# Performance work log

Hardware: AMD Instinct MI355X
Metric: run time of the kernel (lower is better)

The kernel has to match this reference:

```python
import jax, jax.numpy as jnp
import numpy as np
from jax.ops import segment_sum, segment_max

DIM = 64
NUM_FEAT = 14
EDGE_FEAT = 4
OUT_DIM = 16
NUM_GRAPHS = 512
NEG_SLOPE = 0.01


def _leaky(v):
    return jnp.where(v >= 0, v, NEG_SLOPE * v)


def setup_inputs() -> dict:
    key = jax.random.key(0)
    ks = jax.random.split(key, 24)
    N, E = 20000, 40000
    s = 0.1
    inp = {
        "x": jax.random.normal(ks[0], (N, NUM_FEAT), jnp.float32),
        "edge_attr": jax.random.normal(ks[1], (E, EDGE_FEAT), jnp.float32),
        "edge_index": jax.random.randint(ks[2], (2, E), 0, N, jnp.int64) if jax.config.jax_enable_x64 else jax.random.randint(ks[2], (2, E), 0, N).astype(jnp.int32),
        "batch": jnp.sort(jax.random.randint(ks[3], (N,), 0, NUM_GRAPHS)).astype(jnp.int32),
        # lin0
        "lin0_w": s * jax.random.normal(ks[4], (DIM, NUM_FEAT), jnp.float32),
        "lin0_b": s * jax.random.normal(ks[5], (DIM,), jnp.float32),
        # edge network: Linear(4,dim) -> LeakyReLU -> Linear(dim, dim*dim)
        "net_w1": s * jax.random.normal(ks[6], (DIM, EDGE_FEAT), jnp.float32),
        "net_b1": s * jax.random.normal(ks[7], (DIM,), jnp.float32),
        "net_w2": s * jax.random.normal(ks[8], (DIM * DIM, DIM), jnp.float32),
        "net_b2": s * jax.random.normal(ks[9], (DIM * DIM,), jnp.float32),
        # NNConv root weight + bias
        "root_w": s * jax.random.normal(ks[10], (DIM, DIM), jnp.float32),
        "conv_b": s * jax.random.normal(ks[11], (DIM,), jnp.float32),
        # GRU (torch gate order: r, z, n)
        "gru_w_ih": s * jax.random.normal(ks[12], (3 * DIM, DIM), jnp.float32),
        "gru_w_hh": s * jax.random.normal(ks[13], (3 * DIM, DIM), jnp.float32),
        "gru_b_ih": s * jax.random.normal(ks[14], (3 * DIM,), jnp.float32),
        "gru_b_hh": s * jax.random.normal(ks[15], (3 * DIM,), jnp.float32),
        # Set2Set LSTM (input 2*dim, hidden dim; torch gate order: i, f, g, o)
        "lstm_w_ih": s * jax.random.normal(ks[16], (4 * DIM, 2 * DIM), jnp.float32),
        "lstm_w_hh": s * jax.random.normal(ks[17], (4 * DIM, DIM), jnp.float32),
        "lstm_b_ih": s * jax.random.normal(ks[18], (4 * DIM,), jnp.float32),
        "lstm_b_hh": s * jax.random.normal(ks[19], (4 * DIM,), jnp.float32),
        # lin_out
        "lout_w": s * jax.random.normal(ks[20], (OUT_DIM, 2 * DIM), jnp.float32),
        "lout_b": s * jax.random.normal(ks[21], (OUT_DIM,), jnp.float32),
    }
    return inp


def _forward(x, edge_attr, lin0_w, lin0_b, net_w1, net_b1, net_w2, net_b2,
             root_w, conv_b, gru_w_ih, gru_w_hh, gru_b_ih, gru_b_hh,
             lstm_w_ih, lstm_w_hh, lstm_b_ih, lstm_b_hh, lout_w, lout_b,
             edge_index, batch):
    N = x.shape[0]
    src, tgt = edge_index[0], edge_index[1]

    # per-edge dim x dim weight (shared across the 6 steps; edge_attr is static)
    ew = _leaky(edge_attr @ net_w1.T + net_b1) @ net_w2.T + net_b2  # [E, dim*dim]
    ew = ew.reshape(-1, DIM, DIM)  # [E, in, out]

    deg = segment_sum(jnp.ones_like(tgt, jnp.float32), tgt, num_segments=N)
    inv_deg = 1.0 / jnp.maximum(deg, 1.0)

    out = _leaky(x @ lin0_w.T + lin0_b)  # [N, dim]
    h = out
    for _ in range(6):
        msg = jnp.einsum('ed,edo->eo', out[src], ew)  # gather + per-edge matvec
        agg = segment_sum(msg, tgt, num_segments=N) * inv_deg[:, None]  # scatter-mean
        conv = agg + out @ root_w + conv_b
        m = _leaky(conv)
        # GRU cell (seq len 1)
        gi = m @ gru_w_ih.T + gru_b_ih
        gh = h @ gru_w_hh.T + gru_b_hh
        gi_r, gi_z, gi_n = jnp.split(gi, 3, axis=-1)
        gh_r, gh_z, gh_n = jnp.split(gh, 3, axis=-1)
        r = jax.nn.sigmoid(gi_r + gh_r)
        z = jax.nn.sigmoid(gi_z + gh_z)
        n = jnp.tanh(gi_n + r * gh_n)
        h = (1.0 - z) * n + z * h
        out = h

    # Set2Set, processing_steps=1
    B = NUM_GRAPHS
    q_star = jnp.zeros((B, 2 * DIM), x.dtype)
    h_l = jnp.zeros((B, DIM), x.dtype)
    c_l = jnp.zeros((B, DIM), x.dtype)
    gates = q_star @ lstm_w_ih.T + lstm_b_ih + h_l @ lstm_w_hh.T + lstm_b_hh
    gi_, gf_, gg_, go_ = jnp.split(gates, 4, axis=-1)
    i_g = jax.nn.sigmoid(gi_)
    f_g = jax.nn.sigmoid(gf_)
    g_g = jnp.tanh(gg_)
    o_g = jax.nn.sigmoid(go_)
    c = f_g * c_l + i_g * g_g
    q = o_g * jnp.tanh(c)  # [B, dim]

    e = jnp.sum(out * q[batch], axis=-1)  # [N]
    emax = segment_max(e, batch, num_segments=B)
    emax = jnp.where(jnp.isfinite(emax), emax, 0.0)
    ex = jnp.exp(e - emax[batch])
    denom = segment_sum(ex, batch, num_segments=B)
    a = ex / jnp.maximum(denom, 1e-16)[batch]
    r_read = segment_sum(a[:, None] * out, batch, num_segments=B)  # [B, dim]
    q_star = jnp.concatenate([q, r_read], axis=-1)  # [B, 2*dim]

    return q_star @ lout_w.T + lout_b  # [B, out_dim]


def reference(x, edge_attr, edge_index, batch, lin0_w, lin0_b, net_w1, net_b1,
              net_w2, net_b2, root_w, conv_b, gru_w_ih, gru_w_hh, gru_b_ih,
              gru_b_hh, lstm_w_ih, lstm_w_hh, lstm_b_ih, lstm_b_hh, lout_w, lout_b):
    return _forward(x, edge_attr, lin0_w, lin0_b, net_w1, net_b1, net_w2, net_b2,
                    root_w, conv_b, gru_w_ih, gru_w_hh, gru_b_ih, gru_b_hh,
                    lstm_w_ih, lstm_w_hh, lstm_b_ih, lstm_b_hh, lout_w, lout_b,
                    edge_index, batch)
```

## Files before the change

### kernel.cpp

```cpp
#include <hip/hip_runtime.h>
#include <math.h>

#define DIM 64
#define NFEAT 14
#define EFEAT 4
#define ODIM 16
#define NGRAPH 512
#define NEG 0.01f
#define EBLK 160
#define DSPLIT 2

typedef _Float16 f16;
typedef _Float16 f16x8 __attribute__((ext_vector_type(8)));
typedef float f32x4 __attribute__((ext_vector_type(4)));

#define MFMA(a,b,c) __builtin_amdgcn_mfma_f32_16x16x32_f16(a,b,c,0,0,0)

__device__ __forceinline__ float leaky(float v){ return v >= 0.f ? v : NEG*v; }
__device__ __forceinline__ float sigm(float v){ return 1.f/(1.f+expf(-v)); }

__global__ void k_pack(const float* __restrict__ src, f16* __restrict__ dst, int NC, int transB){
    int i = blockIdx.x*blockDim.x + threadIdx.x;
    if (i >= NC*64) return;
    int j = i & 7, l = (i >> 3) & 63, s = (i >> 9) & 1, CT = i >> 10;
    int k = ((l >> 4) << 3) + 32*s + j;
    int c = CT*16 + (l & 15);
    float v = transB ? src[(size_t)k*NC + c] : src[(size_t)c*64 + k];
    dst[i] = (f16)v;
}

__global__ void k_hid(const float* __restrict__ ea, const float* __restrict__ w1,
                      const float* __restrict__ b1, f16* __restrict__ hid16, int E){
    int i = blockIdx.x*blockDim.x + threadIdx.x;
    if (i >= E*DIM) return;
    int e = i >> 6, k = i & 63;
    const float* a = ea + (size_t)e*EFEAT;
    const float* w = w1 + k*EFEAT;
    float v = b1[k] + a[0]*w[0] + a[1]*w[1] + a[2]*w[2] + a[3]*w[3];
    hid16[i] = (f16)leaky(v);
}

__global__ void k_deg(const int* __restrict__ ei, float* __restrict__ deg, int E){
    int e = blockIdx.x*blockDim.x + threadIdx.x;
    if (e < E) atomicAdd(&deg[ei[E + e]], 1.0f);
}

__global__ void k_invdeg(float* __restrict__ deg, int N){
    int i = blockIdx.x*blockDim.x + threadIdx.x;
    if (i < N) deg[i] = 1.0f / fmaxf(deg[i], 1.0f);
}

__global__ void k_lin0(const float* __restrict__ x, const float* __restrict__ w,
                       const float* __restrict__ b, float* __restrict__ hf,
                       f16* __restrict__ out16, int N){
    int i = blockIdx.x*blockDim.x + threadIdx.x;
    if (i >= N*DIM) return;
    int n = i >> 6, o = i & 63;
    const float* xr = x + (size_t)n*NFEAT;
    const float* wr = w + o*NFEAT;
    float v = b[o];
#pragma unroll
    for (int f = 0; f < NFEAT; ++f) v += xr[f]*wr[f];
    v = leaky(v);
    hf[i] = v; out16[i] = (f16)v;
}

__global__ __launch_bounds__(256) void k_nbias(const f16x8* __restrict__ out16v,
                                               const f16x8* __restrict__ b2f,
                                               float* __restrict__ nb, int N){
    int n0 = blockIdx.x*64;
    int tid = threadIdx.x, w = tid >> 6, l = tid & 63, li = l & 15, lh = l >> 4;
    int ar = n0 + 16*w + li;
    f16x8 a0{}, a1{};
    if (ar < N){ a0 = out16v[(size_t)ar*8 + lh]; a1 = out16v[(size_t)ar*8 + lh + 4]; }
    f32x4 z = {0.f,0.f,0.f,0.f};
#pragma unroll
    for (int ct = 0; ct < 4; ++ct){
        f32x4 p = MFMA(a0, b2f[(ct*2+0)*64 + l], z);
        p = MFMA(a1, b2f[(ct*2+1)*64 + l], p);
#pragma unroll
        for (int reg = 0; reg < 4; ++reg){
            int n = n0 + 16*w + lh*4 + reg;
            if (n < N) nb[(size_t)n*64 + ct*16 + li] = p[reg];
        }
    }
}

__global__ __launch_bounds__(320) void k_fmsg(const float* __restrict__ hf,
                                              const f16x8* __restrict__ hid16v,
                                              const f16x8* __restrict__ wpf,
                                              const float* __restrict__ nb,
                                              const int* __restrict__ ei,
                                              float* __restrict__ agg, int E){
    __shared__ f16x8 Wch[2][2048];
    __shared__ f16 OsT[32][168];
    __shared__ int ssrc[EBLK];
    __shared__ int stgt[EBLK];
    int tid = threadIdx.x;
    int e0 = blockIdx.x*EBLK;
    int dz = blockIdx.y;
    int dbase = dz*32;
    if (tid < EBLK){
        int e = e0 + tid;
        ssrc[tid] = (e < E) ? ei[e] : -1;
        stgt[tid] = (e < E) ? ei[E + e] : -1;
    }
    __syncthreads();
    for (int i = tid; i < EBLK*32; i += 320){
        int r = i % EBLK, dl = i / EBLK;
        int s = ssrc[r];
        OsT[dl][r] = (s >= 0) ? (f16)hf[(size_t)s*64 + dbase + dl] : (f16)0.f;
    }
    int w = tid >> 6, l = tid & 63, li = l & 15, lh = l >> 4;
    f16x8 a[2][2];
#pragma unroll
    for (int rt = 0; rt < 2; ++rt){
        int e = e0 + w*32 + rt*16 + li;
        if (e < E){
            a[rt][0] = hid16v[(size_t)e*8 + lh];
            a[rt][1] = hid16v[(size_t)e*8 + lh + 4];
        } else { a[rt][0] = f16x8{}; a[rt][1] = f16x8{}; }
    }
    {
        const f16x8* wsrc0 = wpf + (size_t)dbase*512;
        for (int i = tid; i < 2048; i += 320) Wch[0][i] = wsrc0[i];
    }
    f32x4 acc[2][4] = {};
    __syncthreads();

    for (int c = 0; c < 8; ++c){
        int cb = c & 1;
        f16x8 p0{},p1{},p2{},p3{},p4{},p5{},p6{};
        if (c < 7){
            const f16x8* src = wpf + (size_t)(dbase + (c+1)*4)*512;
            p0 = src[tid];
            p1 = src[tid + 320];
            p2 = src[tid + 640];
            p3 = src[tid + 960];
            p4 = src[tid + 1280];
            p5 = src[tid + 1600];
            if (tid < 128) p6 = src[tid + 1920];
        }
#pragma unroll
        for (int dd = 0; dd < 4; ++dd){
            int dl = c*4 + dd;
            f16 s0 = OsT[dl][w*32 + li];
            f16 s1 = OsT[dl][w*32 + 16 + li];
            f16x8 as00 = a[0][0]*s0, as01 = a[0][1]*s0;
            f16x8 as10 = a[1][0]*s1, as11 = a[1][1]*s1;
#pragma unroll
            for (int ct = 0; ct < 4; ++ct){
                f16x8 b0 = Wch[cb][(dd*8 + ct*2 + 0)*64 + l];
                f16x8 b1 = Wch[cb][(dd*8 + ct*2 + 1)*64 + l];
                acc[0][ct] = MFMA(as00, b0, acc[0][ct]);
                acc[0][ct] = MFMA(as01, b1, acc[0][ct]);
                acc[1][ct] = MFMA(as10, b0, acc[1][ct]);
                acc[1][ct] = MFMA(as11, b1, acc[1][ct]);
            }
        }
        if (c < 7){
            __syncthreads();
            int nb2 = cb ^ 1;
            Wch[nb2][tid]        = p0;
            Wch[nb2][tid + 320]  = p1;
            Wch[nb2][tid + 640]  = p2;
            Wch[nb2][tid + 960]  = p3;
            Wch[nb2][tid + 1280] = p4;
            Wch[nb2][tid + 1600] = p5;
            if (tid < 128) Wch[nb2][tid + 1920] = p6;
            __syncthreads();
        }
    }

#pragma unroll
    for (int rt = 0; rt < 2; ++rt){
#pragma unroll
        for (int reg = 0; reg < 4; ++reg){
            int row = w*32 + rt*16 + lh*4 + reg;
            int t = stgt[row];
            if (t < 0) continue;
            int s = ssrc[row];
#pragma unroll
            for (int ct = 0; ct < 4; ++ct){
                int col = ct*16 + li;
                float v = acc[rt][ct][reg];
                if (dz == 0) v += nb[(size_t)s*64 + col];
                atomicAdd(&agg[(size_t)t*64 + col], v);
            }
        }
    }
}

__global__ __launch_bounds__(256) void k_node(float* __restrict__ hf,
                                              f16* __restrict__ out16,
                                              const f16x8* __restrict__ out16v,
                                              float* __restrict__ agg,
                                              const float* __restrict__ invdeg,
                                              const float* __restrict__ convb,
                                              const f16x8* __restrict__ wrf,
                                              const f16x8* __restrict__ wihf,
                                              const f16x8* __restrict__ whhf,
                                              const float* __restrict__ bih,
                                              const float* __restrict__ bhh,
                                              const f16x8* __restrict__ b2f,
                                              float* __restrict__ nb, int N){
    __shared__ f16 Ms[64][72];
    int n0 = blockIdx.x*64;
    int tid = threadIdx.x, w = tid >> 6, l = tid & 63, li = l & 15, lh = l >> 4;
    f32x4 z = {0.f,0.f,0.f,0.f};

    int ar = n0 + 16*w + li;
    f16x8 a0{}, a1{};
    if (ar < N){ a0 = out16v[(size_t)ar*8 + lh]; a1 = out16v[(size_t)ar*8 + lh + 4]; }

    int nrow[4]; float invd[4];
#pragma unroll
    for (int reg = 0; reg < 4; ++reg){
        nrow[reg] = n0 + 16*w + lh*4 + reg;
        invd[reg] = (nrow[reg] < N) ? invdeg[nrow[reg]] : 0.f;
    }

#pragma unroll
    for (int ct = 0; ct < 4; ++ct){
        f32x4 p = MFMA(a0, wrf[(ct*2+0)*64 + l], z);
        p = MFMA(a1, wrf[(ct*2+1)*64 + l], p);
        int col = ct*16 + li;
        float cb = convb[col];
#pragma unroll
        for (int reg = 0; reg < 4; ++reg){
            int n = nrow[reg];
            float m = 0.f;
            if (n < N){
                size_t idx = (size_t)n*64 + col;
                m = leaky(p[reg] + agg[idx]*invd[reg] + cb);
                agg[idx] = 0.f;
            }
            Ms[16*w + lh*4 + reg][col] = (f16)m;
        }
    }
    __syncthreads();

    f16x8 am0 = *(const f16x8*)&Ms[16*w + li][lh*8];
    f16x8 am1 = *(const f16x8*)&Ms[16*w + li][lh*8 + 32];

#pragma unroll
    for (int ctq = 0; ctq < 4; ++ctq){
        int col = ctq*16 + li;
        f32x4 pir = MFMA(am0, wihf[((ctq+0)*2+0)*64 + l], z);
        pir = MFMA(am1, wihf[((ctq+0)*2+1)*64 + l], pir);
        f32x4 piz = MFMA(am0, wihf[((ctq+4)*2+0)*64 + l], z);
        piz = MFMA(am1, wihf[((ctq+4)*2+1)*64 + l], piz);
        f32x4 pin = MFMA(am0, wihf[((ctq+8)*2+0)*64 + l], z);
        pin = MFMA(am1, wihf[((ctq+8)*2+1)*64 + l], pin);
        f32x4 phr = MFMA(a0, whhf[((ctq+0)*2+0)*64 + l], z);
        phr = MFMA(a1, whhf[((ctq+0)*2+1)*64 + l], phr);
        f32x4 phz = MFMA(a0, whhf[((ctq+4)*2+0)*64 + l], z);
        phz = MFMA(a1, whhf[((ctq+4)*2+1)*64 + l], phz);
        f32x4 phn = MFMA(a0, whhf[((ctq+8)*2+0)*64 + l], z);
        phn = MFMA(a1, whhf[((ctq+8)*2+1)*64 + l], phn);
        float bir = bih[col], biz = bih[64+col], bin = bih[128+col];
        float bhr = bhh[col], bhz = bhh[64+col], bhn = bhh[128+col];
        __syncthreads();
#pragma unroll
        for (int reg = 0; reg < 4; ++reg){
            int n = nrow[reg];
            float hnew = 0.f;
            if (n < N){
                float hv = hf[(size_t)n*64 + col];
                float r  = sigm(pir[reg] + bir + phr[reg] + bhr);
                float zz = sigm(piz[reg] + biz + phz[reg] + bhz);
                float nn = tanhf(pin[reg] + bin + r*(phn[reg] + bhn));
                hnew = (1.f - zz)*nn + zz*hv;
                hf[(size_t)n*64 + col] = hnew;
                out16[(size_t)n*64 + col] = (f16)hnew;
            }
            Ms[16*w + lh*4 + reg][col] = (f16)hnew;
        }
    }
    __syncthreads();

    f16x8 an0 = *(const f16x8*)&Ms[16*w + li][lh*8];
    f16x8 an1 = *(const f16x8*)&Ms[16*w + li][lh*8 + 32];
#pragma unroll
    for (int ct = 0; ct < 4; ++ct){
        f32x4 p = MFMA(an0, b2f[(ct*2+0)*64 + l], z);
        p = MFMA(an1, b2f[(ct*2+1)*64 + l], p);
#pragma unroll
        for (int reg = 0; reg < 4; ++reg){
            int n = nrow[reg];
            if (n < N) nb[(size_t)n*64 + ct*16 + li] = p[reg];
        }
    }
}

__global__ void k_q(const float* __restrict__ bih, const float* __restrict__ bhh,
                    float* __restrict__ q){
    int j = threadIdx.x;
    if (j >= 64) return;
    float gi = bih[j]       + bhh[j];
    float gg = bih[128+j]   + bhh[128+j];
    float go = bih[192+j]   + bhh[192+j];
    float c = sigm(gi)*tanhf(gg);
    q[j] = sigm(go)*tanhf(c);
}

__device__ __forceinline__ unsigned fkey(float f){
    unsigned u = __float_as_uint(f);
    return (u >> 31) ? ~u : (u | 0x80000000u);
}

__global__ void k_edot(const float* __restrict__ out, const float* __restrict__ q,
                       const int* __restrict__ batch, float* __restrict__ ebuf,
                       unsigned* __restrict__ emaxk, int N){
    int gw = (blockIdx.x*blockDim.x + threadIdx.x) >> 6;
    int d = threadIdx.x & 63;
    if (gw >= N) return;
    float v = out[(size_t)gw*64 + d] * q[d];
#pragma unroll
    for (int s = 32; s; s >>= 1) v += __shfl_xor(v, s, 64);
    if (d == 0){
        ebuf[gw] = v;
        atomicMax(&emaxk[batch[gw]], fkey(v));
    }
}

__global__ void k_ex(float* __restrict__ ebuf, const unsigned* __restrict__ emaxk,
                     const int* __restrict__ batch, float* __restrict__ denom, int N){
    int n = blockIdx.x*blockDim.x + threadIdx.x;
    if (n >= N) return;
    int b = batch[n];
    unsigned k = emaxk[b];
    float em = (k == 0u) ? 0.f
             : ((k >> 31) ? __uint_as_float(k ^ 0x80000000u) : __uint_as_float(~k));
    float ex = expf(ebuf[n] - em);
    ebuf[n] = ex;
    atomicAdd(&denom[b], ex);
}

__global__ void k_rr(const float* __restrict__ out, const float* __restrict__ ebuf,
                     const float* __restrict__ denom, const int* __restrict__ batch,
                     float* __restrict__ rr, int N){
    int gw = (blockIdx.x*blockDim.x + threadIdx.x) >> 6;
    int o = threadIdx.x & 63;
    if (gw >= N) return;
    int b = batch[gw];
    float a = ebuf[gw] / fmaxf(denom[b], 1e-16f);
    atomicAdd(&rr[(size_t)b*64 + o], a * out[(size_t)gw*64 + o]);
}

__global__ void k_out(const float* __restrict__ q, const float* __restrict__ rr,
                      const float* __restrict__ lw, const float* __restrict__ lb,
                      float* __restrict__ dout){
    int i = blockIdx.x*blockDim.x + threadIdx.x;
    if (i >= NGRAPH*ODIM) return;
    int b = i / ODIM, j = i % ODIM;
    const float* w = lw + j*128;
    float acc = lb[j];
#pragma unroll 8
    for (int d = 0; d < 64; ++d) acc += w[d]*q[d];
    const float* rb = rr + (size_t)b*64;
#pragma unroll 8
    for (int d = 0; d < 64; ++d) acc += w[64+d]*rb[d];
    dout[i] = acc;
}

extern "C" void kernel_launch(void* const* d_in, const int* in_sizes, int n_in,
                              void* d_out, int out_size, void* d_ws, size_t ws_size,
                              hipStream_t stream){
    const float* x     = (const float*)d_in[0];
    const float* ea    = (const float*)d_in[1];
    const int*   ei    = (const int*)  d_in[2];
    const int*   batch = (const int*)  d_in[3];
    const float* lin0w = (const float*)d_in[4];
    const float* lin0b = (const float*)d_in[5];
    const float* w1    = (const float*)d_in[6];
    const float* b1    = (const float*)d_in[7];
    const float* w2    = (const float*)d_in[8];
    const float* b2    = (const float*)d_in[9];
    const float* rootw = (const float*)d_in[10];
    const float* convb = (const float*)d_in[11];
    const float* gwih  = (const float*)d_in[12];
    const float* gwhh  = (const float*)d_in[13];
    const float* gbih  = (const float*)d_in[14];
    const float* gbhh  = (const float*)d_in[15];
    const float* lsbih = (const float*)d_in[18];
    const float* lsbhh = (const float*)d_in[19];
    const float* loutw = (const float*)d_in[20];
    const float* loutb = (const float*)d_in[21];

    int N = in_sizes[0] / NFEAT;
    int E = in_sizes[1] / EFEAT;

    char* p = (char*)d_ws;
    size_t off = 0;
    auto carve = [&](size_t bytes) -> void* {
        void* r = p + off;
        off += (bytes + 255) & ~(size_t)255;
        return r;
    };
    f16*      hid16  = (f16*)     carve((size_t)E*64*2);
    float*    hf     = (float*)   carve((size_t)N*64*4);
    f16*      out16  = (f16*)     carve((size_t)N*64*2);
    float*    nb     = (float*)   carve((size_t)N*64*4);
    float*    qv     = (float*)   carve(64*4);
    float*    ebuf   = (float*)   carve((size_t)N*4);
    f16*      wpf    = (f16*)     carve((size_t)4096*64*2);
    f16*      wrf    = (f16*)     carve(64*64*2);
    f16*      b2f    = (f16*)     carve(64*64*2);
    f16*      wihf   = (f16*)     carve(192*64*2);
    f16*      whhf   = (f16*)     carve(192*64*2);
    size_t zero_beg = off;
    float*    agg    = (float*)   carve((size_t)N*64*4);
    float*    invdeg = (float*)   carve((size_t)N*4);
    unsigned* emaxk  = (unsigned*)carve(NGRAPH*4);
    float*    denom  = (float*)   carve(NGRAPH*4);
    float*    rr     = (float*)   carve((size_t)NGRAPH*64*4);
    size_t zero_end = off;

    hipMemsetAsync(p + zero_beg, 0, zero_end - zero_beg, stream);

    k_pack<<<(4096*64 + 255)/256, 256, 0, stream>>>(w2,    wpf,  4096, 0);
    k_pack<<<(64*64   + 255)/256, 256, 0, stream>>>(rootw, wrf,  64,   1);
    k_pack<<<(64*64   + 255)/256, 256, 0, stream>>>(b2,    b2f,  64,   1);
    k_pack<<<(192*64  + 255)/256, 256, 0, stream>>>(gwih,  wihf, 192,  0);
    k_pack<<<(192*64  + 255)/256, 256, 0, stream>>>(gwhh,  whhf, 192,  0);

    k_hid<<<((size_t)E*64 + 255)/256, 256, 0, stream>>>(ea, w1, b1, hid16, E);
    k_deg<<<(E + 255)/256, 256, 0, stream>>>(ei, invdeg, E);
    k_invdeg<<<(N + 255)/256, 256, 0, stream>>>(invdeg, N);
    k_lin0<<<((size_t)N*64 + 255)/256, 256, 0, stream>>>(x, lin0w, lin0b, hf, out16, N);

    int eb  = (E + EBLK - 1)/EBLK;
    int nbk = (N + 63)/64;
    int node_grid = ((size_t)N*64 + 255)/256;

    k_nbias<<<nbk, 256, 0, stream>>>((const f16x8*)out16, (const f16x8*)b2f, nb, N);
    for (int it = 0; it < 6; ++it){
        k_fmsg<<<dim3(eb, DSPLIT), 320, 0, stream>>>(hf, (const f16x8*)hid16,
                                                     (const f16x8*)wpf, nb, ei, agg, E);
        k_node<<<nbk, 256, 0, stream>>>(hf, out16, (const f16x8*)out16, agg, invdeg,
                                        convb, (const f16x8*)wrf, (const f16x8*)wihf,
                                        (const f16x8*)whhf, gbih, gbhh,
                                        (const f16x8*)b2f, nb, N);
    }

    k_q<<<1, 64, 0, stream>>>(lsbih, lsbhh, qv);
    k_edot<<<node_grid, 256, 0, stream>>>(hf, qv, batch, ebuf, emaxk, N);
    k_ex<<<(N + 255)/256, 256, 0, stream>>>(ebuf, emaxk, batch, denom, N);
    k_rr<<<node_grid, 256, 0, stream>>>(hf, ebuf, denom, batch, rr, N);
    k_out<<<(NGRAPH*ODIM + 255)/256, 256, 0, stream>>>(qv, rr, loutw, loutb, (float*)d_out);
}
```

Baseline: 568.1 us.

## Shrink edge block to 128, single-buffer weight LDS, drop node-kernel barriers

The message kernel now processes 128 edges per 256-thread block instead of 160 per 320. It replaces the double-buffered weight tile in shared memory with a single buffer filled from register prefetch, and transposes the source-feature staging layout. Halving weight LDS usage is meant to let more blocks fit per CU, at the cost of an extra barrier per chunk. The node kernel also drops its __syncthreads between writing and reading the Ms tile. Each wave appears to read only its own 16 rows, so this may be safe, but removing the barrier inside the gate loop lets a lane overwrite Ms while other lanes may still be reading it.

```diff
diff --git a/kernel.cpp b/kernel.cpp
--- a/kernel.cpp
+++ b/kernel.cpp
@@ -7,7 +7,7 @@
 #define ODIM 16
 #define NGRAPH 512
 #define NEG 0.01f
-#define EBLK 160
+#define EBLK 128
 #define DSPLIT 2
 
 typedef _Float16 f16;
@@ -86,31 +86,31 @@
     }
 }
 
-__global__ __launch_bounds__(320) void k_fmsg(const float* __restrict__ hf,
+__global__ __launch_bounds__(256) void k_fmsg(const float* __restrict__ hf,
                                               const f16x8* __restrict__ hid16v,
                                               const f16x8* __restrict__ wpf,
                                               const float* __restrict__ nb,
                                               const int* __restrict__ ei,
                                               float* __restrict__ agg, int E){
-    __shared__ f16x8 Wch[2][2048];
-    __shared__ f16 OsT[32][168];
+    __shared__ f16x8 Wlds[2048];
+    __shared__ f16 OsT[EBLK][36];
     __shared__ int ssrc[EBLK];
     __shared__ int stgt[EBLK];
     int tid = threadIdx.x;
     int e0 = blockIdx.x*EBLK;
-    int dz = blockIdx.y;
-    int dbase = dz*32;
+    int dbase = blockIdx.y*32;
     if (tid < EBLK){
         int e = e0 + tid;
         ssrc[tid] = (e < E) ? ei[e] : -1;
         stgt[tid] = (e < E) ? ei[E + e] : -1;
     }
     __syncthreads();
-    for (int i = tid; i < EBLK*32; i += 320){
-        int r = i % EBLK, dl = i / EBLK;
+    for (int i = tid; i < EBLK*32; i += 256){
+        int r = i >> 5, dl = i & 31;
         int s = ssrc[r];
-        OsT[dl][r] = (s >= 0) ? (f16)hf[(size_t)s*64 + dbase + dl] : (f16)0.f;
-    }
+        OsT[r][dl] = (s >= 0) ? (f16)hf[(size_t)s*64 + dbase + dl] : (f16)0.f;
+    }
+
     int w = tid >> 6, l = tid & 63, li = l & 15, lh = l >> 4;
     f16x8 a[2][2];
 #pragma unroll
@@ -121,55 +121,43 @@
             a[rt][1] = hid16v[(size_t)e*8 + lh + 4];
         } else { a[rt][0] = f16x8{}; a[rt][1] = f16x8{}; }
     }
+
+    f16x8 p[8];
     {
-        const f16x8* wsrc0 = wpf + (size_t)dbase*512;
-        for (int i = tid; i < 2048; i += 320) Wch[0][i] = wsrc0[i];
-    }
+        const f16x8* src = wpf + (size_t)dbase*512;
+#pragma unroll
+        for (int i = 0; i < 8; ++i) p[i] = src[tid + i*256];
+    }
+
     f32x4 acc[2][4] = {};
-    __syncthreads();
 
     for (int c = 0; c < 8; ++c){
-        int cb = c & 1;
-        f16x8 p0{},p1{},p2{},p3{},p4{},p5{},p6{};
+        __syncthreads();
+#pragma unroll
+        for (int i = 0; i < 8; ++i) Wlds[tid + i*256] = p[i];
+        __syncthreads();
         if (c < 7){
             const f16x8* src = wpf + (size_t)(dbase + (c+1)*4)*512;
-            p0 = src[tid];
-            p1 = src[tid + 320];
-            p2 = src[tid + 640];
-            p3 = src[tid + 960];
-            p4 = src[tid + 1280];
-            p5 = src[tid + 1600];
-            if (tid < 128) p6 = src[tid + 1920];
+#pragma unroll
+            for (int i = 0; i < 8; ++i) p[i] = src[tid + i*256];
         }
 #pragma unroll
         for (int dd = 0; dd < 4; ++dd){
             int dl = c*4 + dd;
-            f16 s0 = OsT[dl][w*32 + li];
-            f16 s1 = OsT[dl][w*32 + 16 + li];
+            f16 s0 = OsT[w*32 + li][dl];
+            f16 s1 = OsT[w*32 + 16 + li][dl];
             f16x8 as00 = a[0][0]*s0, as01 = a[0][1]*s0;
             f16x8 as10 = a[1][0]*s1, as11 = a[1][1]*s1;
 #pragma unroll
             for (int ct = 0; ct < 4; ++ct){
-                f16x8 b0 = Wch[cb][(dd*8 + ct*2 + 0)*64 + l];
-                f16x8 b1 = Wch[cb][(dd*8 + ct*2 + 1)*64 + l];
+                f16x8 b0 = Wlds[(dd*8 + ct*2 + 0)*64 + l];
+                f16x8 b1 = Wlds[(dd*8 + ct*2 + 1)*64 + l];
                 acc[0][ct] = MFMA(as00, b0, acc[0][ct]);
                 acc[0][ct] = MFMA(as01, b1, acc[0][ct]);
                 acc[1][ct] = MFMA(as10, b0, acc[1][ct]);
                 acc[1][ct] = MFMA(as11, b1, acc[1][ct]);
             }
         }
-        if (c < 7){
-            __syncthreads();
-            int nb2 = cb ^ 1;
-            Wch[nb2][tid]        = p0;
-            Wch[nb2][tid + 320]  = p1;
-            Wch[nb2][tid + 640]  = p2;
-            Wch[nb2][tid + 960]  = p3;
-            Wch[nb2][tid + 1280] = p4;
-            Wch[nb2][tid + 1600] = p5;
-            if (tid < 128) Wch[nb2][tid + 1920] = p6;
-            __syncthreads();
-        }
     }
 
 #pragma unroll
@@ -184,7 +172,7 @@
             for (int ct = 0; ct < 4; ++ct){
                 int col = ct*16 + li;
                 float v = acc[rt][ct][reg];
-                if (dz == 0) v += nb[(size_t)s*64 + col];
+                if (blockIdx.y == 0) v += nb[(size_t)s*64 + col];
                 atomicAdd(&agg[(size_t)t*64 + col], v);
             }
         }
@@ -238,7 +226,6 @@
             Ms[16*w + lh*4 + reg][col] = (f16)m;
         }
     }
-    __syncthreads();
 
     f16x8 am0 = *(const f16x8*)&Ms[16*w + li][lh*8];
     f16x8 am1 = *(const f16x8*)&Ms[16*w + li][lh*8 + 32];
@@ -260,7 +247,6 @@
         phn = MFMA(a1, whhf[((ctq+8)*2+1)*64 + l], phn);
         float bir = bih[col], biz = bih[64+col], bin = bih[128+col];
         float bhr = bhh[col], bhz = bhh[64+col], bhn = bhh[128+col];
-        __syncthreads();
 #pragma unroll
         for (int reg = 0; reg < 4; ++reg){
             int n = nrow[reg];
@@ -277,7 +263,6 @@
             Ms[16*w + lh*4 + reg][col] = (f16)hnew;
         }
     }
-    __syncthreads();
 
     f16x8 an0 = *(const f16x8*)&Ms[16*w + li][lh*8];
     f16x8 an1 = *(const f16x8*)&Ms[16*w + li][lh*8 + 32];
@@ -436,7 +421,7 @@
 
     k_nbias<<<nbk, 256, 0, stream>>>((const f16x8*)out16, (const f16x8*)b2f, nb, N);
     for (int it = 0; it < 6; ++it){
-        k_fmsg<<<dim3(eb, DSPLIT), 320, 0, stream>>>(hf, (const f16x8*)hid16,
+        k_fmsg<<<dim3(eb, DSPLIT), 256, 0, stream>>>(hf, (const f16x8*)hid16,
                                                      (const f16x8*)wpf, nb, ei, agg, E);
         k_node<<<nbk, 256, 0, stream>>>(hf, out16, (const f16x8*)out16, agg, invdeg,
                                         convb, (const f16x8*)wrf, (const f16x8*)wihf,
```

Result: faster. 496.8 us (-12.6%).
